# Kernel optimization log

Hardware: AMD Instinct MI355X
Metric: run time of the kernel (lower is better)

Reference implementation:

```python
import jax, jax.numpy as jnp
import numpy as np

B, C, H, W = 32, 64, 64, 64
K, D = 512, 64  # num_embeddings, embedding_dim (C == D)


def setup_inputs() -> dict:
    key = jax.random.key(0)
    k1, k2 = jax.random.split(key)
    z_e = jax.random.normal(k1, (B, C, H, W), dtype=jnp.float32)
    # torch init: uniform_(-1/K, 1/K)
    codebook = jax.random.uniform(k2, (K, D), dtype=jnp.float32,
                                  minval=-1.0 / K, maxval=1.0 / K)
    return {"z_e": z_e, "codebook": codebook}


def reference(z_e, codebook):
    # [B,C,H,W] -> [B,H,W,C] -> [N,C]
    z_flat = jnp.transpose(z_e, (0, 2, 3, 1)).reshape(-1, z_e.shape[1])
    distances = (jnp.sum(z_flat ** 2, axis=1, keepdims=True)
                 + jnp.sum(codebook ** 2, axis=1)
                 - 2.0 * jnp.matmul(z_flat, codebook.T))
    encoding_indices = jnp.argmin(distances, axis=1)  # [N]
    z_q_flat = codebook[encoding_indices]             # [N,D]
    # NOTE: original torch code does z_q_flat.view(z_e.shape) WITHOUT
    # inverse permute; replicate that raw reinterpretation exactly.
    z_q = z_q_flat.reshape(z_e.shape)
    return z_q, encoding_indices
```

## Files before the change

kernel.cpp:

```cpp
#include <hip/hip_runtime.h>


typedef __attribute__((ext_vector_type(4))) float fl4;

__global__ __launch_bounds__(256)
void vq13a(const float* __restrict__ z, float* __restrict__ ow)
{
    __shared__ float zl[256][65];
    const int tid = threadIdx.x;
    const int n0  = blockIdx.x << 8;
    const int n   = n0 + tid;
    const size_t base = (size_t)(n >> 12) * 262144 + (size_t)(n & 4095);

    float p[8];
    #pragma unroll
    for (int c = 0; c < 64; ++c) {
        const float v = z[base + (size_t)c * 4096];
        zl[tid][c] = v;
        const float sq = __fmul_rn(v, v);
        if (c < 8) p[c] = sq;
        else       p[c & 7] = __fadd_rn(p[c & 7], sq);
    }
    const float s1 = __fadd_rn(__fadd_rn(__fadd_rn(p[0],p[1]),__fadd_rn(p[2],p[3])),
                               __fadd_rn(__fadd_rn(p[4],p[5]),__fadd_rn(p[6],p[7])));
    ow[8388608 + n] = s1;
    __syncthreads();

    float* zt = ow + (size_t)n0 * 64;
    #pragma unroll
    for (int j = 0; j < 16; ++j) {
        const int f  = j * 256 + tid;
        const int nl = f >> 4, c0 = (f & 15) << 2;
        fl4 v;
        #pragma unroll
        for (int e = 0; e < 4; ++e) v[e] = zl[nl][c0 + e];
        *(fl4*)(zt + ((size_t)f << 2)) = v;
    }
}

#define CBE(i) cbv[(i) >> 2][(i) & 3]

__global__ __launch_bounds__(512, 4)
void vq13b(const float* __restrict__ cb,
           const float* __restrict__ zt,
           const float* __restrict__ s1g,
           float* __restrict__ ow)
{
    __shared__ float s1l[128];
    __shared__ float cdl[8][128];
    __shared__ int   ckl[8][128];
    __shared__ int   ifin[128];

    const int tid  = threadIdx.x;
    const int w    = tid >> 6;
    const int lane = tid & 63;
    const int n0   = blockIdx.x << 7;
    const int k    = (w << 6) + lane;

    fl4 cbv[16];
    {
        const fl4* rp = (const fl4*)(cb + ((size_t)k << 6));
        #pragma unroll
        for (int j = 0; j < 16; ++j) cbv[j] = rp[j];
    }
    float s2k;
    {
        float q[8];
        #pragma unroll
        for (int j = 0; j < 8; ++j) q[j] = __fmul_rn(CBE(j), CBE(j));
        #pragma unroll
        for (int m = 1; m < 8; ++m)
            #pragma unroll
            for (int j = 0; j < 8; ++j) {
                const float v = CBE(m * 8 + j);
                q[j] = __fadd_rn(q[j], __fmul_rn(v, v));
            }
        s2k = __fadd_rn(__fadd_rn(__fadd_rn(q[0],q[1]),__fadd_rn(q[2],q[3])),
                        __fadd_rn(__fadd_rn(q[4],q[5]),__fadd_rn(q[6],q[7])));
    }

    if (tid < 128) s1l[tid] = s1g[n0 + tid];
    __syncthreads();

    for (int s = 0; s < 128; ++s) {
        const float* zr = zt + ((size_t)(n0 + s) << 6);
        float m = 0.0f;
        #pragma unroll
        for (int c = 0; c < 64; ++c)
            m = fmaf(zr[c], CBE(c), m);
        const float T = __fadd_rn(s1l[s], s2k);
        const float d = __fsub_rn(T, 2.0f * m);

        float dm = d;
        #pragma unroll
        for (int off = 1; off < 64; off <<= 1)
            dm = fminf(dm, __shfl_xor(dm, off, 64));
        const unsigned long long eq = __ballot(d == dm);
        if (lane == 0) {
            cdl[w][s] = dm;
            ckl[w][s] = (w << 6) + (__ffsll((long long)eq) - 1);
        }
    }
    __syncthreads();

    if (tid < 128) {
        float bd = cdl[0][tid]; int bk = ckl[0][tid];
        #pragma unroll
        for (int ww = 1; ww < 8; ++ww) {
            const float dw = cdl[ww][tid];
            const int   kw = ckl[ww][tid];
            if (dw < bd) { bd = dw; bk = kw; }
        }
        ifin[tid] = bk;
        ow[8388608 + n0 + tid] = (float)bk;
    }
    __syncthreads();

    float* ob = ow + ((size_t)n0 << 6);
    #pragma unroll
    for (int it = 0; it < 4; ++it) {
        const int o    = it * 2048 + (tid << 2);
        const int sloc = o >> 6;
        const int c0   = o & 63;
        const int idx  = ifin[sloc] & 511;
        const fl4 v = *(const fl4*)(cb + ((size_t)idx << 6) + c0);
        *(fl4*)(ob + o) = v;
    }
}

extern "C" void kernel_launch(void* const* d_in, const int* in_sizes, int n_in,
                              void* d_out, int out_size, void* d_ws, size_t ws_size,
                              hipStream_t stream) {
    const float* z  = (const float*)d_in[0];
    const float* cb = (const float*)d_in[1];
    float* out = (float*)d_out;
    vq13a<<<512, 256, 0, stream>>>(z, out);
    vq13b<<<1024, 512, 0, stream>>>(cb, out, out + 8388608, out);
}
```

Measured before the change: 264.4 us.

## Vectorize transpose loads and block distance loop over four rows with prefetch

The transpose kernel now reads z with float4 loads along the spatial dimension and stages it in a channel-major LDS tile, computing partial squared norms per channel group and combining them through shared memory. The distance kernel processes four z rows per iteration with double-buffered float4 loads, interleaving loads and FMAs to raise ILP and cut per-row scalar load overhead. This costs more vector registers and changes the sum order for s1, which may shift argmin ties.

Result: slower. 321.3 us (+21.5%).

```diff
diff --git a/kernel.cpp b/kernel.cpp
--- a/kernel.cpp
+++ b/kernel.cpp
@@ -4,36 +4,58 @@
 typedef __attribute__((ext_vector_type(4))) float fl4;
 
 __global__ __launch_bounds__(256)
-void vq13a(const float* __restrict__ z, float* __restrict__ ow)
+void vq14a(const float* __restrict__ z, float* __restrict__ ow)
 {
-    __shared__ float zl[256][65];
+    __shared__ fl4   zl4[64][64];
+    __shared__ float pl[8][256];
+
     const int tid = threadIdx.x;
     const int n0  = blockIdx.x << 8;
-    const int n   = n0 + tid;
-    const size_t base = (size_t)(n >> 12) * 262144 + (size_t)(n & 4095);
-
-    float p[8];
-    #pragma unroll
-    for (int c = 0; c < 64; ++c) {
-        const float v = z[base + (size_t)c * 4096];
-        zl[tid][c] = v;
-        const float sq = __fmul_rn(v, v);
-        if (c < 8) p[c] = sq;
-        else       p[c & 7] = __fadd_rn(p[c & 7], sq);
-    }
-    const float s1 = __fadd_rn(__fadd_rn(__fadd_rn(p[0],p[1]),__fadd_rn(p[2],p[3])),
-                               __fadd_rn(__fadd_rn(p[4],p[5]),__fadd_rn(p[6],p[7])));
-    ow[8388608 + n] = s1;
-    __syncthreads();
-
-    float* zt = ow + (size_t)n0 * 64;
+    const int cq  = tid >> 6;
+    const int s4g = tid & 63;
+    const size_t zb = (size_t)(n0 >> 12) * 262144 + (size_t)(n0 & 4095)
+                    + ((size_t)s4g << 2);
+
+    float pq[4], pq4[4];
     #pragma unroll
     for (int j = 0; j < 16; ++j) {
-        const int f  = j * 256 + tid;
-        const int nl = f >> 4, c0 = (f & 15) << 2;
+        const int c = cq + (j << 2);
+        const fl4 v = *(const fl4*)(z + zb + (size_t)c * 4096);
+        zl4[c][s4g] = v;
+        #pragma unroll
+        for (int e = 0; e < 4; ++e) {
+            const float sq = __fmul_rn(v[e], v[e]);
+            if (j == 0)            pq[e]  = sq;
+            else if (j == 1)       pq4[e] = sq;
+            else if ((j & 1) == 0) pq[e]  = __fadd_rn(pq[e],  sq);
+            else                   pq4[e] = __fadd_rn(pq4[e], sq);
+        }
+    }
+    #pragma unroll
+    for (int e = 0; e < 4; ++e) {
+        pl[cq][(s4g << 2) + e]     = pq[e];
+        pl[cq + 4][(s4g << 2) + e] = pq4[e];
+    }
+    __syncthreads();
+
+    {
+        const int s = tid;
+        const float s1 = __fadd_rn(
+            __fadd_rn(__fadd_rn(pl[0][s], pl[1][s]), __fadd_rn(pl[2][s], pl[3][s])),
+            __fadd_rn(__fadd_rn(pl[4][s], pl[5][s]), __fadd_rn(pl[6][s], pl[7][s])));
+        ow[8388608 + n0 + s] = s1;
+    }
+
+    float* zt = ow + ((size_t)n0 << 6);
+    #pragma unroll
+    for (int it = 0; it < 16; ++it) {
+        const int f  = (it << 8) + tid;
+        const int nl = f >> 4;
+        const int c0 = (f & 15) << 2;
         fl4 v;
         #pragma unroll
-        for (int e = 0; e < 4; ++e) v[e] = zl[nl][c0 + e];
+        for (int e = 0; e < 4; ++e)
+            v[e] = zl4[c0 + e][nl >> 2][nl & 3];
         *(fl4*)(zt + ((size_t)f << 2)) = v;
     }
 }
@@ -41,7 +63,7 @@
 #define CBE(i) cbv[(i) >> 2][(i) & 3]
 
 __global__ __launch_bounds__(512, 4)
-void vq13b(const float* __restrict__ cb,
+void vq14b(const float* __restrict__ cb,
            const float* __restrict__ zt,
            const float* __restrict__ s1g,
            float* __restrict__ ow)
@@ -75,31 +97,72 @@
                 const float v = CBE(m * 8 + j);
                 q[j] = __fadd_rn(q[j], __fmul_rn(v, v));
             }
-        s2k = __fadd_rn(__fadd_rn(__fadd_rn(q[0],q[1]),__fadd_rn(q[2],q[3])),
-                        __fadd_rn(__fadd_rn(q[4],q[5]),__fadd_rn(q[6],q[7])));
+        s2k = __fadd_rn(__fadd_rn(__fadd_rn(q[0], q[1]), __fadd_rn(q[2], q[3])),
+                        __fadd_rn(__fadd_rn(q[4], q[5]), __fadd_rn(q[6], q[7])));
     }
 
     if (tid < 128) s1l[tid] = s1g[n0 + tid];
     __syncthreads();
 
-    for (int s = 0; s < 128; ++s) {
-        const float* zr = zt + ((size_t)(n0 + s) << 6);
-        float m = 0.0f;
-        #pragma unroll
-        for (int c = 0; c < 64; ++c)
-            m = fmaf(zr[c], CBE(c), m);
-        const float T = __fadd_rn(s1l[s], s2k);
-        const float d = __fsub_rn(T, 2.0f * m);
-
-        float dm = d;
-        #pragma unroll
-        for (int off = 1; off < 64; off <<= 1)
-            dm = fminf(dm, __shfl_xor(dm, off, 64));
-        const unsigned long long eq = __ballot(d == dm);
-        if (lane == 0) {
-            cdl[w][s] = dm;
-            ckl[w][s] = (w << 6) + (__ffsll((long long)eq) - 1);
-        }
+#define LOADC(B, C4) do {                                         \
+        B##0 = *(const fl4*)(zr0 + ((C4) << 2));                  \
+        B##1 = *(const fl4*)(zr1 + ((C4) << 2));                  \
+        B##2 = *(const fl4*)(zr2 + ((C4) << 2));                  \
+        B##3 = *(const fl4*)(zr3 + ((C4) << 2)); } while (0)
+#define FMAC(B, C4) do {                                          \
+        _Pragma("unroll")                                         \
+        for (int e = 0; e < 4; ++e) {                             \
+            const float cbe = CBE(((C4) << 2) + e);               \
+            a0 = fmaf(B##0[e], cbe, a0);                          \
+            a1 = fmaf(B##1[e], cbe, a1);                          \
+            a2 = fmaf(B##2[e], cbe, a2);                          \
+            a3 = fmaf(B##3[e], cbe, a3); } } while (0)
+#define REDUCE(DI, SI) do {                                       \
+        float dm = (DI);                                          \
+        _Pragma("unroll")                                         \
+        for (int off = 1; off < 64; off <<= 1)                    \
+            dm = fminf(dm, __shfl_xor(dm, off, 64));              \
+        const unsigned long long eq = __ballot((DI) == dm);       \
+        if (lane == 0) {                                          \
+            cdl[w][s0 + (SI)] = dm;                               \
+            ckl[w][s0 + (SI)] = (w << 6) + (int)__ffsll((long long)eq) - 1; } } while (0)
+
+    for (int sb = 0; sb < 32; ++sb) {
+        const int s0 = sb << 2;
+        const float* zr0 = zt + ((size_t)(n0 + s0) << 6);
+        const float* zr1 = zr0 + 64;
+        const float* zr2 = zr0 + 128;
+        const float* zr3 = zr0 + 192;
+
+        float a0 = 0.0f, a1 = 0.0f, a2 = 0.0f, a3 = 0.0f;
+        fl4 x0, x1, x2, x3, y0, y1, y2, y3;
+        LOADC(x, 0);
+        LOADC(y, 1);  FMAC(x, 0);
+        LOADC(x, 2);  FMAC(y, 1);
+        LOADC(y, 3);  FMAC(x, 2);
+        LOADC(x, 4);  FMAC(y, 3);
+        LOADC(y, 5);  FMAC(x, 4);
+        LOADC(x, 6);  FMAC(y, 5);
+        LOADC(y, 7);  FMAC(x, 6);
+        LOADC(x, 8);  FMAC(y, 7);
+        LOADC(y, 9);  FMAC(x, 8);
+        LOADC(x, 10); FMAC(y, 9);
+        LOADC(y, 11); FMAC(x, 10);
+        LOADC(x, 12); FMAC(y, 11);
+        LOADC(y, 13); FMAC(x, 12);
+        LOADC(x, 14); FMAC(y, 13);
+        LOADC(y, 15); FMAC(x, 14);
+                      FMAC(y, 15);
+
+        const float d0 = __fsub_rn(__fadd_rn(s1l[s0 + 0], s2k), 2.0f * a0);
+        const float d1 = __fsub_rn(__fadd_rn(s1l[s0 + 1], s2k), 2.0f * a1);
+        const float d2 = __fsub_rn(__fadd_rn(s1l[s0 + 2], s2k), 2.0f * a2);
+        const float d3 = __fsub_rn(__fadd_rn(s1l[s0 + 3], s2k), 2.0f * a3);
+
+        REDUCE(d0, 0);
+        REDUCE(d1, 1);
+        REDUCE(d2, 2);
+        REDUCE(d3, 3);
     }
     __syncthreads();
 
@@ -134,6 +197,6 @@
     const float* z  = (const float*)d_in[0];
     const float* cb = (const float*)d_in[1];
     float* out = (float*)d_out;
-    vq13a<<<512, 256, 0, stream>>>(z, out);
-    vq13b<<<1024, 512, 0, stream>>>(cb, out, out + 8388608, out);
+    vq14a<<<512, 256, 0, stream>>>(z, out);
+    vq14b<<<1024, 512, 0, stream>>>(cb, out, out + 8388608, out);
 }
```

## Hand-write distance loop in inline assembly with scalar z loads and swizzle reduction

Applied to the files above, without the earlier changes.

Replaces the compiler-generated inner distance loop with inline GCN assembly. The codebook row is pinned in fixed vector registers, each z row is loaded into scalar registers with s_load_dwordx16 so the FMAs take scalar operands, and the wave min is reduced with ds_swizzle plus a bpermute. The aim is to cut instruction overhead and per-lane redundant loads of the shared z row. It removes the occupancy hint from launch bounds, hardcodes register numbers that could clash with compiler allocation, and serializes each swizzle step behind a waitcnt.

Measured after the change: 410.0 us. +55.1%, slower.

```diff
diff --git a/kernel.cpp b/kernel.cpp
--- a/kernel.cpp
+++ b/kernel.cpp
@@ -4,7 +4,7 @@
 typedef __attribute__((ext_vector_type(4))) float fl4;
 
 __global__ __launch_bounds__(256)
-void vq13a(const float* __restrict__ z, float* __restrict__ ow)
+void vq16a(const float* __restrict__ z, float* __restrict__ ow)
 {
     __shared__ float zl[256][65];
     const int tid = threadIdx.x;
@@ -38,10 +38,8 @@
     }
 }
 
-#define CBE(i) cbv[(i) >> 2][(i) & 3]
-
-__global__ __launch_bounds__(512, 4)
-void vq13b(const float* __restrict__ cb,
+__global__ __launch_bounds__(512)
+void vq16b(const float* __restrict__ cb,
            const float* __restrict__ zt,
            const float* __restrict__ s1g,
            float* __restrict__ ow)
@@ -57,24 +55,17 @@
     const int n0   = blockIdx.x << 7;
     const int k    = (w << 6) + lane;
 
-    fl4 cbv[16];
-    {
-        const fl4* rp = (const fl4*)(cb + ((size_t)k << 6));
-        #pragma unroll
-        for (int j = 0; j < 16; ++j) cbv[j] = rp[j];
-    }
     float s2k;
     {
+        const float* row = cb + ((size_t)k << 6);
         float q[8];
         #pragma unroll
-        for (int j = 0; j < 8; ++j) q[j] = __fmul_rn(CBE(j), CBE(j));
+        for (int j = 0; j < 8; ++j) q[j] = __fmul_rn(row[j], row[j]);
         #pragma unroll
         for (int m = 1; m < 8; ++m)
             #pragma unroll
-            for (int j = 0; j < 8; ++j) {
-                const float v = CBE(m * 8 + j);
-                q[j] = __fadd_rn(q[j], __fmul_rn(v, v));
-            }
+            for (int j = 0; j < 8; ++j)
+                q[j] = __fadd_rn(q[j], __fmul_rn(row[m*8+j], row[m*8+j]));
         s2k = __fadd_rn(__fadd_rn(__fadd_rn(q[0],q[1]),__fadd_rn(q[2],q[3])),
                         __fadd_rn(__fadd_rn(q[4],q[5]),__fadd_rn(q[6],q[7])));
     }
@@ -82,25 +73,132 @@
     if (tid < 128) s1l[tid] = s1g[n0 + tid];
     __syncthreads();
 
-    for (int s = 0; s < 128; ++s) {
-        const float* zr = zt + ((size_t)(n0 + s) << 6);
-        float m = 0.0f;
-        #pragma unroll
-        for (int c = 0; c < 64; ++c)
-            m = fmaf(zr[c], CBE(c), m);
-        const float T = __fadd_rn(s1l[s], s2k);
-        const float d = __fsub_rn(T, 2.0f * m);
-
-        float dm = d;
-        #pragma unroll
-        for (int off = 1; off < 64; off <<= 1)
-            dm = fminf(dm, __shfl_xor(dm, off, 64));
-        const unsigned long long eq = __ballot(d == dm);
-        if (lane == 0) {
-            cdl[w][s] = dm;
-            ckl[w][s] = (w << 6) + (__ffsll((long long)eq) - 1);
-        }
-    }
+    const float* cbrow = cb + ((size_t)k << 6);
+    const float* zrow  = zt + ((size_t)n0 << 6);
+    unsigned s1a = (unsigned)(unsigned long long)&s1l[0];
+    unsigned cda = (unsigned)(unsigned long long)&cdl[w][0];
+    unsigned cka = (unsigned)(unsigned long long)&ckl[w][0];
+    const int x32a  = (lane ^ 32) << 2;
+    const int wbase = w << 6;
+
+    asm volatile(
+        "global_load_dwordx4 v[64:67],   %[cbr], off\n\t"
+        "global_load_dwordx4 v[68:71],   %[cbr], off offset:16\n\t"
+        "global_load_dwordx4 v[72:75],   %[cbr], off offset:32\n\t"
+        "global_load_dwordx4 v[76:79],   %[cbr], off offset:48\n\t"
+        "global_load_dwordx4 v[80:83],   %[cbr], off offset:64\n\t"
+        "global_load_dwordx4 v[84:87],   %[cbr], off offset:80\n\t"
+        "global_load_dwordx4 v[88:91],   %[cbr], off offset:96\n\t"
+        "global_load_dwordx4 v[92:95],   %[cbr], off offset:112\n\t"
+        "global_load_dwordx4 v[96:99],   %[cbr], off offset:128\n\t"
+        "global_load_dwordx4 v[100:103], %[cbr], off offset:144\n\t"
+        "global_load_dwordx4 v[104:107], %[cbr], off offset:160\n\t"
+        "global_load_dwordx4 v[108:111], %[cbr], off offset:176\n\t"
+        "global_load_dwordx4 v[112:115], %[cbr], off offset:192\n\t"
+        "global_load_dwordx4 v[116:119], %[cbr], off offset:208\n\t"
+        "global_load_dwordx4 v[120:123], %[cbr], off offset:224\n\t"
+        "global_load_dwordx4 v[124:127], %[cbr], off offset:240\n\t"
+        "s_mov_b64 s[34:35], %[zrow]\n\t"
+        "s_movk_i32 s26, 0x80\n\t"
+        "s_waitcnt vmcnt(0)\n\t"
+        "1:\n\t"
+        "s_load_dwordx16 s[36:51], s[34:35], 0x0\n\t"
+        "s_load_dwordx16 s[52:67], s[34:35], 0x40\n\t"
+        "s_load_dwordx16 s[68:83], s[34:35], 0x80\n\t"
+        "s_load_dwordx16 s[84:99], s[34:35], 0xC0\n\t"
+        "ds_read_b32 v41, %[s1a]\n\t"
+        "v_mov_b32 v40, 0\n\t"
+        "s_waitcnt lgkmcnt(0)\n\t"
+        "v_fmac_f32 v40, s36, v64\n\t"  "v_fmac_f32 v40, s37, v65\n\t"
+        "v_fmac_f32 v40, s38, v66\n\t"  "v_fmac_f32 v40, s39, v67\n\t"
+        "v_fmac_f32 v40, s40, v68\n\t"  "v_fmac_f32 v40, s41, v69\n\t"
+        "v_fmac_f32 v40, s42, v70\n\t"  "v_fmac_f32 v40, s43, v71\n\t"
+        "v_fmac_f32 v40, s44, v72\n\t"  "v_fmac_f32 v40, s45, v73\n\t"
+        "v_fmac_f32 v40, s46, v74\n\t"  "v_fmac_f32 v40, s47, v75\n\t"
+        "v_fmac_f32 v40, s48, v76\n\t"  "v_fmac_f32 v40, s49, v77\n\t"
+        "v_fmac_f32 v40, s50, v78\n\t"  "v_fmac_f32 v40, s51, v79\n\t"
+        "v_fmac_f32 v40, s52, v80\n\t"  "v_fmac_f32 v40, s53, v81\n\t"
+        "v_fmac_f32 v40, s54, v82\n\t"  "v_fmac_f32 v40, s55, v83\n\t"
+        "v_fmac_f32 v40, s56, v84\n\t"  "v_fmac_f32 v40, s57, v85\n\t"
+        "v_fmac_f32 v40, s58, v86\n\t"  "v_fmac_f32 v40, s59, v87\n\t"
+        "v_fmac_f32 v40, s60, v88\n\t"  "v_fmac_f32 v40, s61, v89\n\t"
+        "v_fmac_f32 v40, s62, v90\n\t"  "v_fmac_f32 v40, s63, v91\n\t"
+        "v_fmac_f32 v40, s64, v92\n\t"  "v_fmac_f32 v40, s65, v93\n\t"
+        "v_fmac_f32 v40, s66, v94\n\t"  "v_fmac_f32 v40, s67, v95\n\t"
+        "v_fmac_f32 v40, s68, v96\n\t"  "v_fmac_f32 v40, s69, v97\n\t"
+        "v_fmac_f32 v40, s70, v98\n\t"  "v_fmac_f32 v40, s71, v99\n\t"
+        "v_fmac_f32 v40, s72, v100\n\t" "v_fmac_f32 v40, s73, v101\n\t"
+        "v_fmac_f32 v40, s74, v102\n\t" "v_fmac_f32 v40, s75, v103\n\t"
+        "v_fmac_f32 v40, s76, v104\n\t" "v_fmac_f32 v40, s77, v105\n\t"
+        "v_fmac_f32 v40, s78, v106\n\t" "v_fmac_f32 v40, s79, v107\n\t"
+        "v_fmac_f32 v40, s80, v108\n\t" "v_fmac_f32 v40, s81, v109\n\t"
+        "v_fmac_f32 v40, s82, v110\n\t" "v_fmac_f32 v40, s83, v111\n\t"
+        "v_fmac_f32 v40, s84, v112\n\t" "v_fmac_f32 v40, s85, v113\n\t"
+        "v_fmac_f32 v40, s86, v114\n\t" "v_fmac_f32 v40, s87, v115\n\t"
+        "v_fmac_f32 v40, s88, v116\n\t" "v_fmac_f32 v40, s89, v117\n\t"
+        "v_fmac_f32 v40, s90, v118\n\t" "v_fmac_f32 v40, s91, v119\n\t"
+        "v_fmac_f32 v40, s92, v120\n\t" "v_fmac_f32 v40, s93, v121\n\t"
+        "v_fmac_f32 v40, s94, v122\n\t" "v_fmac_f32 v40, s95, v123\n\t"
+        "v_fmac_f32 v40, s96, v124\n\t" "v_fmac_f32 v40, s97, v125\n\t"
+        "v_fmac_f32 v40, s98, v126\n\t" "v_fmac_f32 v40, s99, v127\n\t"
+        "v_add_f32 v41, v41, %[s2k]\n\t"
+        "v_fma_f32 v40, v40, -2.0, v41\n\t"
+        "v_mov_b32 v42, v40\n\t"
+        "ds_swizzle_b32 v43, v42 offset:0x041F\n\t"
+        "s_waitcnt lgkmcnt(0)\n\t"
+        "v_min_f32 v42, v42, v43\n\t"
+        "ds_swizzle_b32 v43, v42 offset:0x081F\n\t"
+        "s_waitcnt lgkmcnt(0)\n\t"
+        "v_min_f32 v42, v42, v43\n\t"
+        "ds_swizzle_b32 v43, v42 offset:0x101F\n\t"
+        "s_waitcnt lgkmcnt(0)\n\t"
+        "v_min_f32 v42, v42, v43\n\t"
+        "ds_swizzle_b32 v43, v42 offset:0x201F\n\t"
+        "s_waitcnt lgkmcnt(0)\n\t"
+        "v_min_f32 v42, v42, v43\n\t"
+        "ds_swizzle_b32 v43, v42 offset:0x401F\n\t"
+        "s_waitcnt lgkmcnt(0)\n\t"
+        "v_min_f32 v42, v42, v43\n\t"
+        "ds_bpermute_b32 v43, %[x32], v42\n\t"
+        "s_waitcnt lgkmcnt(0)\n\t"
+        "v_min_f32 v42, v42, v43\n\t"
+        "v_cmp_eq_f32 vcc, v40, v42\n\t"
+        "s_ff1_i32_b64 s33, vcc\n\t"
+        "v_add_u32 v44, s33, %[wb]\n\t"
+        "s_mov_b64 s[28:29], exec\n\t"
+        "s_mov_b64 exec, 1\n\t"
+        "ds_write_b32 %[cda], v42\n\t"
+        "ds_write_b32 %[cka], v44\n\t"
+        "s_mov_b64 exec, s[28:29]\n\t"
+        "v_add_u32 %[s1a], 4, %[s1a]\n\t"
+        "v_add_u32 %[cda], 4, %[cda]\n\t"
+        "v_add_u32 %[cka], 4, %[cka]\n\t"
+        "s_add_u32 s34, s34, 0x100\n\t"
+        "s_addc_u32 s35, s35, 0\n\t"
+        "s_sub_i32 s26, s26, 1\n\t"
+        "s_cmp_lg_u32 s26, 0\n\t"
+        "s_cbranch_scc1 1b\n\t"
+        : [s1a] "+v"(s1a), [cda] "+v"(cda), [cka] "+v"(cka)
+        : [cbr] "v"(cbrow), [zrow] "s"(zrow), [s2k] "v"(s2k),
+          [wb] "v"(wbase), [x32] "v"(x32a)
+        : "memory", "vcc", "s26", "s28", "s29", "s33", "s34", "s35",
+          "s36","s37","s38","s39","s40","s41","s42","s43","s44","s45",
+          "s46","s47","s48","s49","s50","s51","s52","s53","s54","s55",
+          "s56","s57","s58","s59","s60","s61","s62","s63","s64","s65",
+          "s66","s67","s68","s69","s70","s71","s72","s73","s74","s75",
+          "s76","s77","s78","s79","s80","s81","s82","s83","s84","s85",
+          "s86","s87","s88","s89","s90","s91","s92","s93","s94","s95",
+          "s96","s97","s98","s99",
+          "v40","v41","v42","v43","v44",
+          "v64","v65","v66","v67","v68","v69","v70","v71",
+          "v72","v73","v74","v75","v76","v77","v78","v79",
+          "v80","v81","v82","v83","v84","v85","v86","v87",
+          "v88","v89","v90","v91","v92","v93","v94","v95",
+          "v96","v97","v98","v99","v100","v101","v102","v103",
+          "v104","v105","v106","v107","v108","v109","v110","v111",
+          "v112","v113","v114","v115","v116","v117","v118","v119",
+          "v120","v121","v122","v123","v124","v125","v126","v127");
+
     __syncthreads();
 
     if (tid < 128) {
@@ -134,6 +232,6 @@
     const float* z  = (const float*)d_in[0];
     const float* cb = (const float*)d_in[1];
     float* out = (float*)d_out;
-    vq13a<<<512, 256, 0, stream>>>(z, out);
-    vq13b<<<1024, 512, 0, stream>>>(cb, out, out + 8388608, out);
+    vq16a<<<512, 256, 0, stream>>>(z, out);
+    vq16b<<<1024, 512, 0, stream>>>(cb, out, out + 8388608, out);
 }
```

## Rewrite distance inner loop in inline asm with LDS-staged z rows

Applied to the files above, without the earlier changes.

Stages the block's 128 z rows into shared memory and replaces the compiler-generated distance loop with hand-written GCN assembly. Each wave processes two samples per iteration with interleaved ds_read_b128 loads and v_fmac chains. The cross-lane argmin uses DPP, swizzle and bpermute instead of shuffles, and lane 0 writes its result with a single masked store. The aim is to cut global/scalar load overhead and reduction latency, at the cost of fragile hardcoded register allocation, 32KB of extra LDS that may reduce occupancy, and a loop count that assumes a fixed tile size.

Result: faster. 251.4 us (-4.9%).

```diff
diff --git a/kernel.cpp b/kernel.cpp
--- a/kernel.cpp
+++ b/kernel.cpp
@@ -4,7 +4,7 @@
 typedef __attribute__((ext_vector_type(4))) float fl4;
 
 __global__ __launch_bounds__(256)
-void vq13a(const float* __restrict__ z, float* __restrict__ ow)
+void vq19a(const float* __restrict__ z, float* __restrict__ ow)
 {
     __shared__ float zl[256][65];
     const int tid = threadIdx.x;
@@ -38,17 +38,40 @@
     }
 }
 
-#define CBE(i) cbv[(i) >> 2][(i) & 3]
+#define FM2(ZA,ZB,C) \
+    "v_fmac_f32 v52, v" #ZA ", v" #C "\n\t" \
+    "v_fmac_f32 v53, v" #ZB ", v" #C "\n\t"
+#define LA4(O0,O1,O2,O3) \
+    "ds_read_b128 v[20:23], %[zb] offset:" #O0 "\n\t" \
+    "ds_read_b128 v[24:27], %[zb] offset:" #O1 "\n\t" \
+    "ds_read_b128 v[28:31], %[zb] offset:" #O2 "\n\t" \
+    "ds_read_b128 v[32:35], %[zb] offset:" #O3 "\n\t"
+#define LB4(O0,O1,O2,O3) \
+    "ds_read_b128 v[36:39], %[zb] offset:" #O0 "\n\t" \
+    "ds_read_b128 v[40:43], %[zb] offset:" #O1 "\n\t" \
+    "ds_read_b128 v[44:47], %[zb] offset:" #O2 "\n\t" \
+    "ds_read_b128 v[48:51], %[zb] offset:" #O3 "\n\t"
+#define FMA_A(C0,C1,C2,C3,C4,C5,C6,C7) \
+    FM2(20,28,C0) FM2(21,29,C1) FM2(22,30,C2) FM2(23,31,C3) \
+    FM2(24,32,C4) FM2(25,33,C5) FM2(26,34,C6) FM2(27,35,C7)
+#define FMA_B(C0,C1,C2,C3,C4,C5,C6,C7) \
+    FM2(36,44,C0) FM2(37,45,C1) FM2(38,46,C2) FM2(39,47,C3) \
+    FM2(40,48,C4) FM2(41,49,C5) FM2(42,50,C6) FM2(43,51,C7)
+#define DPPMIN(MOD) \
+    "v_min_f32 v58, v58, v58 " MOD " row_mask:0xf bank_mask:0xf\n\t" \
+    "v_min_f32 v59, v59, v59 " MOD " row_mask:0xf bank_mask:0xf\n\t" \
+    "s_nop 1\n\t"
 
 __global__ __launch_bounds__(512, 4)
-void vq13b(const float* __restrict__ cb,
+void vq19b(const float* __restrict__ cb,
            const float* __restrict__ zt,
            const float* __restrict__ s1g,
            float* __restrict__ ow)
 {
-    __shared__ float s1l[128];
-    __shared__ float cdl[8][128];
-    __shared__ int   ckl[8][128];
+    __shared__ __align__(16) float zl[8192];
+    __shared__ __align__(16) float s1l[128];
+    __shared__ __align__(16) float cdl[8][128];
+    __shared__ __align__(16) int   ckl[8][128];
     __shared__ int   ifin[128];
 
     const int tid  = threadIdx.x;
@@ -57,50 +80,144 @@
     const int n0   = blockIdx.x << 7;
     const int k    = (w << 6) + lane;
 
-    fl4 cbv[16];
-    {
-        const fl4* rp = (const fl4*)(cb + ((size_t)k << 6));
-        #pragma unroll
-        for (int j = 0; j < 16; ++j) cbv[j] = rp[j];
-    }
     float s2k;
     {
+        const float* row = cb + ((size_t)k << 6);
         float q[8];
         #pragma unroll
-        for (int j = 0; j < 8; ++j) q[j] = __fmul_rn(CBE(j), CBE(j));
+        for (int j = 0; j < 8; ++j) q[j] = __fmul_rn(row[j], row[j]);
         #pragma unroll
         for (int m = 1; m < 8; ++m)
             #pragma unroll
-            for (int j = 0; j < 8; ++j) {
-                const float v = CBE(m * 8 + j);
-                q[j] = __fadd_rn(q[j], __fmul_rn(v, v));
-            }
+            for (int j = 0; j < 8; ++j)
+                q[j] = __fadd_rn(q[j], __fmul_rn(row[m*8+j], row[m*8+j]));
         s2k = __fadd_rn(__fadd_rn(__fadd_rn(q[0],q[1]),__fadd_rn(q[2],q[3])),
                         __fadd_rn(__fadd_rn(q[4],q[5]),__fadd_rn(q[6],q[7])));
     }
 
     if (tid < 128) s1l[tid] = s1g[n0 + tid];
-    __syncthreads();
-
-    for (int s = 0; s < 128; ++s) {
-        const float* zr = zt + ((size_t)(n0 + s) << 6);
-        float m = 0.0f;
-        #pragma unroll
-        for (int c = 0; c < 64; ++c)
-            m = fmaf(zr[c], CBE(c), m);
-        const float T = __fadd_rn(s1l[s], s2k);
-        const float d = __fsub_rn(T, 2.0f * m);
-
-        float dm = d;
-        #pragma unroll
-        for (int off = 1; off < 64; off <<= 1)
-            dm = fminf(dm, __shfl_xor(dm, off, 64));
-        const unsigned long long eq = __ballot(d == dm);
-        if (lane == 0) {
-            cdl[w][s] = dm;
-            ckl[w][s] = (w << 6) + (__ffsll((long long)eq) - 1);
-        }
-    }
+    {
+        const fl4* src = (const fl4*)(zt + ((size_t)n0 << 6));
+        fl4* dst = (fl4*)zl;
+        dst[tid]        = src[tid];
+        dst[512  + tid] = src[512  + tid];
+        dst[1024 + tid] = src[1024 + tid];
+        dst[1536 + tid] = src[1536 + tid];
+    }
+    __syncthreads();
+
+    const float* cbrow = cb + ((size_t)k << 6);
+    unsigned s1a = (unsigned)(unsigned long long)&s1l[0];
+    unsigned cda = (unsigned)(unsigned long long)&cdl[w][0];
+    unsigned cka = (unsigned)(unsigned long long)&ckl[w][0];
+    unsigned zb  = (unsigned)(unsigned long long)&zl[0];
+    const int x32a  = (lane ^ 32) << 2;
+    const int wbase = w << 6;
+
+    asm volatile(
+        "global_load_dwordx4 v[64:67],   %[cbr], off\n\t"
+        "global_load_dwordx4 v[68:71],   %[cbr], off offset:16\n\t"
+        "global_load_dwordx4 v[72:75],   %[cbr], off offset:32\n\t"
+        "global_load_dwordx4 v[76:79],   %[cbr], off offset:48\n\t"
+        "global_load_dwordx4 v[80:83],   %[cbr], off offset:64\n\t"
+        "global_load_dwordx4 v[84:87],   %[cbr], off offset:80\n\t"
+        "global_load_dwordx4 v[88:91],   %[cbr], off offset:96\n\t"
+        "global_load_dwordx4 v[92:95],   %[cbr], off offset:112\n\t"
+        "global_load_dwordx4 v[96:99],   %[cbr], off offset:128\n\t"
+        "global_load_dwordx4 v[100:103], %[cbr], off offset:144\n\t"
+        "global_load_dwordx4 v[104:107], %[cbr], off offset:160\n\t"
+        "global_load_dwordx4 v[108:111], %[cbr], off offset:176\n\t"
+        "global_load_dwordx4 v[112:115], %[cbr], off offset:192\n\t"
+        "global_load_dwordx4 v[116:119], %[cbr], off offset:208\n\t"
+        "global_load_dwordx4 v[120:123], %[cbr], off offset:224\n\t"
+        "global_load_dwordx4 v[124:127], %[cbr], off offset:240\n\t"
+        "s_movk_i32 s33, 64\n\t"
+        "s_waitcnt vmcnt(0)\n\t"
+        "1:\n\t"
+        "v_mov_b32 v52, 0\n\t"
+        "v_mov_b32 v53, 0\n\t"
+        "ds_read_b64 v[54:55], %[s1a]\n\t"
+        LA4(0,16,256,272)
+        LB4(32,48,288,304)
+        "s_waitcnt lgkmcnt(4)\n\t"
+        FMA_A(64,65,66,67,68,69,70,71)
+        LA4(64,80,320,336)
+        "s_waitcnt lgkmcnt(4)\n\t"
+        FMA_B(72,73,74,75,76,77,78,79)
+        LB4(96,112,352,368)
+        "s_waitcnt lgkmcnt(4)\n\t"
+        FMA_A(80,81,82,83,84,85,86,87)
+        LA4(128,144,384,400)
+        "s_waitcnt lgkmcnt(4)\n\t"
+        FMA_B(88,89,90,91,92,93,94,95)
+        LB4(160,176,416,432)
+        "s_waitcnt lgkmcnt(4)\n\t"
+        FMA_A(96,97,98,99,100,101,102,103)
+        LA4(192,208,448,464)
+        "s_waitcnt lgkmcnt(4)\n\t"
+        FMA_B(104,105,106,107,108,109,110,111)
+        LB4(224,240,480,496)
+        "s_waitcnt lgkmcnt(4)\n\t"
+        FMA_A(112,113,114,115,116,117,118,119)
+        "s_waitcnt lgkmcnt(0)\n\t"
+        FMA_B(120,121,122,123,124,125,126,127)
+        "v_add_f32 v54, %[s2k], v54\n\t"
+        "v_add_f32 v55, %[s2k], v55\n\t"
+        "v_fma_f32 v56, v52, -2.0, v54\n\t"
+        "v_fma_f32 v57, v53, -2.0, v55\n\t"
+        "v_mov_b32 v58, v56\n\t"
+        "v_mov_b32 v59, v57\n\t"
+        "s_nop 1\n\t"
+        DPPMIN("quad_perm:[1,0,3,2]")
+        DPPMIN("quad_perm:[2,3,0,1]")
+        DPPMIN("row_half_mirror")
+        DPPMIN("row_mirror")
+        "ds_swizzle_b32 v62, v58 offset:0x401F\n\t"
+        "ds_swizzle_b32 v63, v59 offset:0x401F\n\t"
+        "s_waitcnt lgkmcnt(0)\n\t"
+        "v_min_f32 v58, v58, v62\n\t"
+        "v_min_f32 v59, v59, v63\n\t"
+        "ds_bpermute_b32 v62, %[x32], v58\n\t"
+        "ds_bpermute_b32 v63, %[x32], v59\n\t"
+        "s_waitcnt lgkmcnt(0)\n\t"
+        "v_min_f32 v58, v58, v62\n\t"
+        "v_min_f32 v59, v59, v63\n\t"
+        "v_cmp_eq_f32 vcc, v56, v58\n\t"
+        "s_ff1_i32_b64 s20, vcc\n\t"
+        "v_cmp_eq_f32 vcc, v57, v59\n\t"
+        "s_ff1_i32_b64 s21, vcc\n\t"
+        "v_add_u32 v60, s20, %[wb]\n\t"
+        "v_add_u32 v61, s21, %[wb]\n\t"
+        "s_mov_b64 s[24:25], exec\n\t"
+        "s_mov_b64 exec, 1\n\t"
+        "ds_write_b64 %[cda], v[58:59]\n\t"
+        "ds_write_b64 %[cka], v[60:61]\n\t"
+        "s_mov_b64 exec, s[24:25]\n\t"
+        "v_add_u32 %[s1a], 8, %[s1a]\n\t"
+        "v_add_u32 %[cda], 8, %[cda]\n\t"
+        "v_add_u32 %[cka], 8, %[cka]\n\t"
+        "v_add_u32 %[zb], 0x200, %[zb]\n\t"
+        "s_sub_i32 s33, s33, 1\n\t"
+        "s_cmp_lg_u32 s33, 0\n\t"
+        "s_cbranch_scc1 1b\n\t"
+        : [s1a] "+v"(s1a), [cda] "+v"(cda), [cka] "+v"(cka), [zb] "+v"(zb)
+        : [cbr] "v"(cbrow), [s2k] "v"(s2k), [wb] "v"(wbase), [x32] "v"(x32a)
+        : "memory", "vcc", "s20","s21","s24","s25","s33",
+          "v20","v21","v22","v23","v24","v25","v26","v27",
+          "v28","v29","v30","v31","v32","v33","v34","v35",
+          "v36","v37","v38","v39","v40","v41","v42","v43",
+          "v44","v45","v46","v47","v48","v49","v50","v51",
+          "v52","v53","v54","v55","v56","v57","v58","v59",
+          "v60","v61","v62","v63",
+          "v64","v65","v66","v67","v68","v69","v70","v71",
+          "v72","v73","v74","v75","v76","v77","v78","v79",
+          "v80","v81","v82","v83","v84","v85","v86","v87",
+          "v88","v89","v90","v91","v92","v93","v94","v95",
+          "v96","v97","v98","v99","v100","v101","v102","v103",
+          "v104","v105","v106","v107","v108","v109","v110","v111",
+          "v112","v113","v114","v115","v116","v117","v118","v119",
+          "v120","v121","v122","v123","v124","v125","v126","v127");
+
     __syncthreads();
 
     if (tid < 128) {
@@ -134,6 +251,6 @@
     const float* z  = (const float*)d_in[0];
     const float* cb = (const float*)d_in[1];
     float* out = (float*)d_out;
-    vq13a<<<512, 256, 0, stream>>>(z, out);
-    vq13b<<<1024, 512, 0, stream>>>(cb, out, out + 8388608, out);
+    vq19a<<<512, 256, 0, stream>>>(z, out);
+    vq19b<<<1024, 512, 0, stream>>>(cb, out, out + 8388608, out);
 }
```
